# Performance work log

Measured on AMD Instinct MI355X. Metric: run time of the kernel, lower is better.

Reference implementation:

```python
import jax, jax.numpy as jnp
import numpy as np

GRID_SIZE = 5
SPLINE_ORDER = 3
NUM_BASIS = GRID_SIZE + SPLINE_ORDER  # 8


def _make_grid(in_features):
    # efficient-kan style uniform extended grid over [-1, 1]
    h = 2.0 / GRID_SIZE
    g = jnp.arange(-SPLINE_ORDER, GRID_SIZE + SPLINE_ORDER + 1, dtype=jnp.float32) * h - 1.0
    return jnp.broadcast_to(g, (in_features, g.shape[0]))  # [in, 12]


def _b_splines(x, grid):
    # x: [..., in], grid: [in, G]; returns [..., in, NUM_BASIS] via Cox-de Boor
    xe = x[..., None]
    bases = ((xe >= grid[:, :-1]) & (xe < grid[:, 1:])).astype(x.dtype)
    for k in range(1, SPLINE_ORDER + 1):
        left = (xe - grid[:, :-(k + 1)]) / (grid[:, k:-1] - grid[:, :-(k + 1)]) * bases[..., :-1]
        right = (grid[:, k + 1:] - xe) / (grid[:, k + 1:] - grid[:, 1:-k]) * bases[..., 1:]
        bases = left + right
    return bases


def kan_linear(x, bw, sw):
    # bw: [out, in], sw: [out, in, NUM_BASIS]
    base = jnp.matmul(jax.nn.silu(x), bw.T)
    spl = _b_splines(x, _make_grid(bw.shape[1]))
    spline = jnp.einsum('...ik,oik->...o', spl, sw)
    return base + spline


def kan2(x, bw1, sw1, bw2, sw2):
    return kan_linear(kan_linear(x, bw1, sw1), bw2, sw2)


def _att_matrix(q, bw1, sw1, bw2, sw2):
    n, h = q.shape
    pairs = jnp.concatenate([
        jnp.broadcast_to(q[:, None, :], (n, n, h)),
        jnp.broadcast_to(q[None, :, :], (n, n, h)),
    ], axis=-1)  # [n, n, 2h]
    return kan2(pairs, bw1, sw1, bw2, sw2)[..., 0]  # [n, n]


def setup_inputs() -> dict:
    key = jax.random.key(0)
    ks = jax.random.split(key, 32)
    n, h, m = 384, 32, 50

    def rn(k, shape, s=1.0):
        return jax.random.normal(k, shape, dtype=jnp.float32) * s

    inp = {
        'x': rn(ks[0], (n, h)),
        'y': rn(ks[1], (n, h)),
        'target': rn(ks[2], (n, h)),
        'bias': rn(ks[3], (1,), 0.1),
    }
    i = 4
    for pre in ('x', 'y', 't'):
        din = 2 * h
        inp[pre + '1bw'] = rn(ks[i], (m, din), 0.1)
        inp[pre + '1sw'] = rn(ks[i + 1], (m, din, NUM_BASIS), 0.1)
        inp[pre + '2bw'] = rn(ks[i + 2], (1, m), 0.1)
        inp[pre + '2sw'] = rn(ks[i + 3], (1, m, NUM_BASIS), 0.1)
        i += 4
    inp['f1bw'] = rn(ks[i], (m, 3 * h), 0.1)
    inp['f1sw'] = rn(ks[i + 1], (m, 3 * h, NUM_BASIS), 0.1)
    inp['f2bw'] = rn(ks[i + 2], (3, m), 0.1)
    inp['f2sw'] = rn(ks[i + 3], (3, m, NUM_BASIS), 0.1)
    i += 4
    inp['l1bw'] = rn(ks[i], (h, h), 0.1)
    inp['l1sw'] = rn(ks[i + 1], (h, h, NUM_BASIS), 0.1)
    inp['l2bw'] = rn(ks[i + 2], (h, h), 0.1)
    inp['l2sw'] = rn(ks[i + 3], (h, h, NUM_BASIS), 0.1)
    return inp


def reference(x, y, target, bias,
              x1bw, x1sw, x2bw, x2sw,
              y1bw, y1sw, y2bw, y2sw,
              t1bw, t1sw, t2bw, t2sw,
              f1bw, f1sw, f2bw, f2sw,
              l1bw, l1sw, l2bw, l2sw):
    xA = _att_matrix(x, x1bw, x1sw, x2bw, x2sw)
    yA = _att_matrix(y, y1bw, y1sw, y2bw, y2sw)
    tA = _att_matrix(target, t1bw, t1sw, t2bw, t2sw)

    # dynamic modal fusion weights
    feats = jnp.concatenate([x.mean(0, keepdims=True), y.mean(0, keepdims=True),
                             target.mean(0, keepdims=True)], axis=-1)  # [1, 3h]
    w = jax.nn.softmax(kan2(feats, f1bw, f1sw, f2bw, f2sw), axis=-1)[0]  # [3]

    fusion_att = w[0] * xA + w[1] * yA + w[2] * tA + bias
    fusion_att = jax.nn.softmax(fusion_att, axis=-1)
    target_att = jnp.matmul(fusion_att, target)  # dropout is identity at eval
    y1 = jax.nn.relu(kan_linear(target_att, l1bw, l1sw))
    y2 = jax.nn.relu(kan_linear(y1, l2bw, l2sw))
    return y2
```

## Files before the change

### kernel.cpp

```cpp
#include <hip/hip_runtime.h>

#define NN 384
#define HH 32
#define MM 50

__device__ __forceinline__ float fastRcp(float x) { return __builtin_amdgcn_rcpf(x); }

__device__ __forceinline__ void featEval(float x, float& sil, int& kb, float b[4]) {
  sil = x * fastRcp(1.0f + __expf(-x));
  const float u  = (x + 1.0f) * 2.5f;
  const float fu = floorf(u);
  const bool valid = (fu >= -3.0f) && (fu <= 7.0f);
  const float s = valid ? (1.0f / 6.0f) : 0.0f;
  kb = valid ? (int)fu : 100;
  const float tt = u - fu;
  const float t2 = tt * tt, t3 = t2 * tt, omt = 1.0f - tt;
  b[0] = omt * omt * omt * s;
  b[1] = (3.0f * t3 - 6.0f * t2 + 4.0f) * s;
  b[2] = (-3.0f * t3 + 3.0f * t2 + 3.0f * tt + 1.0f) * s;
  b[3] = t3 * s;
}

__device__ __forceinline__ float waveReduce(float v) {
#pragma unroll
  for (int off = 32; off > 0; off >>= 1) v += __shfl_down(v, off);
  return v;
}

__device__ __forceinline__ float dot4(float4 a, float4 b) {
  float r = a.x * b.x;
  r = fmaf(a.y, b.y, r);
  r = fmaf(a.z, b.z, r);
  r = fmaf(a.w, b.w, r);
  return r;
}

__global__ __launch_bounds__(384) void stageA_kernel(
    const float* __restrict__ x, const float* __restrict__ y, const float* __restrict__ tg,
    const float* __restrict__ xbw, const float* __restrict__ xsw,
    const float* __restrict__ ybw, const float* __restrict__ ysw,
    const float* __restrict__ tbw, const float* __restrict__ tsw,
    const float* __restrict__ f1bw, const float* __restrict__ f1sw,
    const float* __restrict__ f2bw, const float* __restrict__ f2sw,
    float* __restrict__ A, float* __restrict__ Bt, float* __restrict__ wout)
{
  const int tid = threadIdx.x;
  const int lane = tid & 63, w = tid >> 6;
  const int i = blockIdx.x;
  const int m = blockIdx.y;
  const int half = blockIdx.z;

  if (i < NN) {
    __shared__ float bas[HH * 8];
    __shared__ float sil[HH];
    const float* q  = (m == 0) ? x   : ((m == 1) ? y   : tg);
    const float* bw = (m == 0) ? xbw : ((m == 1) ? ybw : tbw);
    const float* sw = (m == 0) ? xsw : ((m == 1) ? ysw : tsw);
    const int cb = half * HH;

    if (tid < HH * 8) bas[tid] = 0.0f;
    __syncthreads();
    if (tid < HH) {
      float b[4]; float s; int kb;
      featEval(q[i * HH + tid], s, kb, b);
      sil[tid] = s;
#pragma unroll
      for (int r = 0; r < 4; ++r) {
        const int k = kb + r;
        if ((unsigned)k < 8u) bas[tid * 8 + k] = b[r];
      }
    }
    __syncthreads();

    const float4* bas4 = (const float4*)bas;
    const float4 bb = bas4[lane];
    const float sl = (lane < HH) ? sil[lane] : 0.0f;
#pragma unroll 2
    for (int o = w; o < MM; o += 6) {
      const float4 wv4 = ((const float4*)(sw + ((size_t)(o * 2 * HH + cb) << 3)))[lane];
      const float bwv = (lane < HH) ? bw[o * 2 * HH + cb + lane] : 0.0f;
      float acc = dot4(wv4, bb);
      acc = fmaf(bwv, sl, acc);
      acc = waveReduce(acc);
      if (lane == 0) {
        if (half == 0) A[((size_t)m * NN + i) * MM + o] = acc;
        else           Bt[((size_t)m * MM + o) * NN + i] = acc;
      }
    }
    return;
  }

  if (m != 0 || half != 0) return;
  {
    __shared__ float4 part4[3][8][16];
    __shared__ float sil96[96];
    __shared__ float bas768[96 * 8];
    __shared__ float z1[MM];
    __shared__ float sil2[MM];
    __shared__ float bas400[MM * 8];
    __shared__ float s3[3];

    {
      const int mm = tid >> 7;
      const int sub = tid & 127;
      const int q4 = sub >> 4;
      const int prt = sub & 15;
      const float* src = (mm == 0) ? x : ((mm == 1) ? y : tg);
      const float4* s4 = (const float4*)src;
      float4 a = make_float4(0.f, 0.f, 0.f, 0.f);
      for (int r = prt; r < NN; r += 16) {
        const float4 v = s4[r * 8 + q4];
        a.x += v.x; a.y += v.y; a.z += v.z; a.w += v.w;
      }
      part4[mm][q4][prt] = a;
    }
    for (int idx = tid; idx < 96 * 8; idx += 384) bas768[idx] = 0.0f;
    for (int idx = tid; idx < MM * 8; idx += 384) bas400[idx] = 0.0f;
    __syncthreads();

    if (tid < 96) {
      const int mm = tid >> 5, col = tid & 31;
      const int q4 = col >> 2, comp = col & 3;
      const float* pp = (const float*)&part4[mm][q4][0];
      float v = 0.0f;
#pragma unroll
      for (int prt = 0; prt < 16; ++prt) v += pp[prt * 4 + comp];
      const float fv = v * (1.0f / NN);
      float b[4]; float s; int kb;
      featEval(fv, s, kb, b);
      sil96[tid] = s;
#pragma unroll
      for (int r = 0; r < 4; ++r) {
        const int k = kb + r;
        if ((unsigned)k < 8u) bas768[tid * 8 + k] = b[r];
      }
    }
    __syncthreads();

    {
      const float4* bas4 = (const float4*)bas768;
      for (int o = w; o < MM; o += 6) {
        const float4* sp4 = (const float4*)(f1sw + (size_t)o * (96 * 8));
        float acc = 0.0f;
#pragma unroll
        for (int r = 0; r < 3; ++r)
          acc += dot4(sp4[lane + 64 * r], bas4[lane + 64 * r]);
#pragma unroll
        for (int r = 0; r < 2; ++r) {
          const int e = lane + 64 * r;
          if (e < 96) acc = fmaf(f1bw[o * 96 + e], sil96[e], acc);
        }
        acc = waveReduce(acc);
        if (lane == 0) z1[o] = acc;
      }
    }
    __syncthreads();

    if (tid < MM) {
      float b[4]; float s; int kb;
      featEval(z1[tid], s, kb, b);
      sil2[tid] = s;
#pragma unroll
      for (int r = 0; r < 4; ++r) {
        const int k = kb + r;
        if ((unsigned)k < 8u) bas400[tid * 8 + k] = b[r];
      }
    }
    __syncthreads();

    if (w < 3) {
      const float4* bas4 = (const float4*)bas400;
      const float4* sp4 = (const float4*)(f2sw + (size_t)w * (MM * 8));
      float acc = 0.0f;
#pragma unroll
      for (int r = 0; r < 2; ++r) {
        const int f = lane + 64 * r;
        if (f < MM * 2) acc += dot4(sp4[f], bas4[f]);
      }
      if (lane < MM) acc = fmaf(f2bw[w * MM + lane], sil2[lane], acc);
      acc = waveReduce(acc);
      if (lane == 0) s3[w] = acc;
    }
    __syncthreads();

    if (tid == 0) {
      const float mx = fmaxf(s3[0], fmaxf(s3[1], s3[2]));
      const float e0 = __expf(s3[0] - mx), e1 = __expf(s3[1] - mx), e2 = __expf(s3[2] - mx);
      const float inv = fastRcp(e0 + e1 + e2);
      wout[0] = e0 * inv; wout[1] = e1 * inv; wout[2] = e2 * inv;
    }
  }
}

__global__ __launch_bounds__(384) void score_kernel(
    const float* __restrict__ A, const float* __restrict__ Bt,
    const float* __restrict__ x2bw, const float* __restrict__ y2bw, const float* __restrict__ t2bw,
    const float* __restrict__ x2sw, const float* __restrict__ y2sw, const float* __restrict__ t2sw,
    float* __restrict__ Sp)
{
  __shared__ float sA[MM];
  __shared__ float sBW[MM];
  __shared__ float4 herm[43];
  __shared__ float4 coefC[MM][43];
  const int tid = threadIdx.x;
  const int i = blockIdx.x;
  const int m = blockIdx.y;
  const float* bsrc = (m == 0) ? x2bw : ((m == 1) ? y2bw : t2bw);
  const float* ssrc = (m == 0) ? x2sw : ((m == 1) ? y2sw : t2sw);

  if (tid < MM) {
    sA[tid]  = A[((size_t)m * NN + i) * MM + tid];
    sBW[tid] = bsrc[tid];
  }
  if (tid >= 64 && tid < 64 + 43) {
    const int c = tid - 64;
    float4 h;
    if (c == 0) {
      h = make_float4(0.f, 0.f, 0.f, 0.f);
    } else if (c == 42) {
      h = make_float4(8.2f, 0.4f, 0.f, 0.f);
    } else {
      const float z0 = -8.2f + (float)(c - 1) * 0.4f;
      const float z1 = z0 + 0.4f;
      const float s0 = fastRcp(1.0f + __expf(-z0));
      const float s1 = fastRcp(1.0f + __expf(-z1));
      const float p0 = z0 * s0, p1 = z1 * s1;
      const float m0 = 0.4f * (s0 * (1.0f + z0 * (1.0f - s0)));
      const float m1 = 0.4f * (s1 * (1.0f + z1 * (1.0f - s1)));
      h.x = p0;
      h.y = m0;
      h.z = 3.0f * (p1 - p0) - 2.0f * m0 - m1;
      h.w = 2.0f * (p0 - p1) + m0 + m1;
    }
    herm[c] = h;
  }
  __syncthreads();

  for (int idx = tid; idx < MM * 43; idx += 384) {
    const int k = idx / 43, cc = idx - k * 43;
    const float bwk = sBW[k];
    const float4 H = herm[cc];
    float4 C = make_float4(bwk * H.x, bwk * H.y, bwk * H.z, bwk * H.w);
    if (cc >= 16 && cc <= 26) {
      const int j = cc - 16;
      float p[4];
#pragma unroll
      for (int r = 0; r < 4; ++r) {
        const int pi = j + r - 3;
        p[r] = ((unsigned)pi < 8u) ? ssrc[k * 8 + pi] : 0.0f;
      }
      C.x += (p[0] + 4.0f * p[1] + p[2]) * (1.0f / 6.0f);
      C.y += (p[2] - p[0]) * 0.5f;
      C.z += (p[0] - 2.0f * p[1] + p[2]) * 0.5f;
      C.w += (p[3] - p[0]) * (1.0f / 6.0f) + (p[1] - p[2]) * 0.5f;
    }
    coefC[k][cc] = C;
  }
  __syncthreads();

#define KAN_EVAL(zz, kk, accv)                                          \
  {                                                                     \
    const float z_ = (zz);                                              \
    const float u_ = fmaf(z_, 2.5f, 20.5f);                             \
    const float fu_ = floorf(u_);                                       \
    const float cu_ = fminf(fmaxf(fu_, -1.0f), 41.0f);                  \
    const float t_ = u_ - cu_;                                          \
    const int cc_ = (int)cu_ + 1;                                       \
    const float4 C_ = coefC[kk][cc_];                                   \
    accv += fmaf(t_, fmaf(t_, fmaf(t_, C_.w, C_.z), C_.y), C_.x);       \
  }

  const float* BtBase = Bt + (size_t)m * MM * NN + tid;
  float acc0 = 0.0f, acc1 = 0.0f;
  float za = BtBase[0];
  float zb = BtBase[NN];
  float zc = BtBase[2 * NN];
  float zd = BtBase[3 * NN];
#pragma unroll 5
  for (int k = 0; k < MM; k += 2) {
    float ze = 0.0f, zf = 0.0f;
    if (k + 5 < MM) {
      ze = BtBase[(size_t)(k + 4) * NN];
      zf = BtBase[(size_t)(k + 5) * NN];
    }
    KAN_EVAL(sA[k] + za,     k,     acc0);
    KAN_EVAL(sA[k + 1] + zb, k + 1, acc1);
    za = zc; zb = zd; zc = ze; zd = zf;
  }
#undef KAN_EVAL

  Sp[((size_t)m * NN + i) * NN + tid] = acc0 + acc1;
}

__global__ __launch_bounds__(384) void row_kernel(
    const float* __restrict__ Sp, const float* __restrict__ wv, const float* __restrict__ bias,
    const float* __restrict__ tg,
    const float* __restrict__ l1bw, const float* __restrict__ l1sw,
    const float* __restrict__ l2bw, const float* __restrict__ l2sw,
    float* __restrict__ out)
{
  __shared__ float p[NN];
  __shared__ float redm[6], reds[6];
  __shared__ float part[12][HH];
  __shared__ float ta[HH];
  __shared__ float basF[HH * 8];
  __shared__ float silF[HH];
  __shared__ float y1v[HH];
  const int tid = threadIdx.x;
  const int lane = tid & 63, w = tid >> 6;
  const int i = blockIdx.x;

  float stot = bias[0];
  stot = fmaf(wv[0], Sp[(size_t)i * NN + tid], stot);
  stot = fmaf(wv[1], Sp[((size_t)NN + i) * NN + tid], stot);
  stot = fmaf(wv[2], Sp[((size_t)2 * NN + i) * NN + tid], stot);

  float v = stot;
#pragma unroll
  for (int off = 32; off > 0; off >>= 1) v = fmaxf(v, __shfl_down(v, off));
  if (lane == 0) redm[w] = v;
  __syncthreads();
  float mx = redm[0];
#pragma unroll
  for (int ww = 1; ww < 6; ++ww) mx = fmaxf(mx, redm[ww]);
  const float e = __expf(stot - mx);
  p[tid] = e;
  float sv = e;
#pragma unroll
  for (int off = 32; off > 0; off >>= 1) sv += __shfl_down(sv, off);
  if (lane == 0) reds[w] = sv;
  __syncthreads();
  const float ssum = reds[0] + reds[1] + reds[2] + reds[3] + reds[4] + reds[5];
  const float inv = 1.0f / ssum;

  const int d = tid & 31, g = tid >> 5;
  float acc2 = 0.0f;
  for (int s2 = 0; s2 < 32; ++s2) {
    const int j = g * 32 + s2;
    acc2 = fmaf(p[j], tg[j * HH + d], acc2);
  }
  part[g][d] = acc2;
  if (tid < HH * 8) basF[tid] = 0.0f;
  __syncthreads();
  if (tid < HH) {
    float a = 0.0f;
#pragma unroll
    for (int gg = 0; gg < 12; ++gg) a += part[gg][tid];
    ta[tid] = a * inv;
  }
  __syncthreads();

  if (tid < HH) {
    float b[4]; float s; int kb;
    featEval(ta[tid], s, kb, b);
    silF[tid] = s;
#pragma unroll
    for (int r = 0; r < 4; ++r) {
      const int k = kb + r;
      if ((unsigned)k < 8u) basF[tid * 8 + k] = b[r];
    }
  }
  __syncthreads();
  {
    const float4 bb = ((const float4*)basF)[lane];
    for (int o = w; o < HH; o += 6) {
      const float4* sp4 = (const float4*)(l1sw + ((size_t)o << 8));
      float acc = dot4(sp4[lane], bb);
      if (lane < HH) acc = fmaf(l1bw[o * HH + lane], silF[lane], acc);
      acc = waveReduce(acc);
      if (lane == 0) y1v[o] = fmaxf(acc, 0.0f);
    }
  }
  __syncthreads();
  if (tid < HH * 8) basF[tid] = 0.0f;
  __syncthreads();
  if (tid < HH) {
    float b[4]; float s; int kb;
    featEval(y1v[tid], s, kb, b);
    silF[tid] = s;
#pragma unroll
    for (int r = 0; r < 4; ++r) {
      const int k = kb + r;
      if ((unsigned)k < 8u) basF[tid * 8 + k] = b[r];
    }
  }
  __syncthreads();
  {
    const float4 bb = ((const float4*)basF)[lane];
    for (int o = w; o < HH; o += 6) {
      const float4* sp4 = (const float4*)(l2sw + ((size_t)o << 8));
      float acc = dot4(sp4[lane], bb);
      if (lane < HH) acc = fmaf(l2bw[o * HH + lane], silF[lane], acc);
      acc = waveReduce(acc);
      if (lane == 0) out[i * HH + o] = fmaxf(acc, 0.0f);
    }
  }
}

extern "C" void kernel_launch(void* const* d_in, const int* in_sizes, int n_in,
                              void* d_out, int out_size, void* d_ws, size_t ws_size,
                              hipStream_t stream)
{
  const float* x    = (const float*)d_in[0];
  const float* y    = (const float*)d_in[1];
  const float* tg   = (const float*)d_in[2];
  const float* bias = (const float*)d_in[3];
  const float* x1bw = (const float*)d_in[4];
  const float* x1sw = (const float*)d_in[5];
  const float* x2bw = (const float*)d_in[6];
  const float* x2sw = (const float*)d_in[7];
  const float* y1bw = (const float*)d_in[8];
  const float* y1sw = (const float*)d_in[9];
  const float* y2bw = (const float*)d_in[10];
  const float* y2sw = (const float*)d_in[11];
  const float* t1bw = (const float*)d_in[12];
  const float* t1sw = (const float*)d_in[13];
  const float* t2bw = (const float*)d_in[14];
  const float* t2sw = (const float*)d_in[15];
  const float* f1bw = (const float*)d_in[16];
  const float* f1sw = (const float*)d_in[17];
  const float* f2bw = (const float*)d_in[18];
  const float* f2sw = (const float*)d_in[19];
  const float* l1bw = (const float*)d_in[20];
  const float* l1sw = (const float*)d_in[21];
  const float* l2bw = (const float*)d_in[22];
  const float* l2sw = (const float*)d_in[23];
  float* out = (float*)d_out;

  float* ws = (float*)d_ws;
  float* A  = ws;
  float* Bt = ws + 3 * NN * MM;
  float* Sp = ws + 6 * NN * MM;
  float* wv = Sp + 3 * NN * NN;

  stageA_kernel<<<dim3(NN + 1, 3, 2), 384, 0, stream>>>(
      x, y, tg, x1bw, x1sw, y1bw, y1sw, t1bw, t1sw,
      f1bw, f1sw, f2bw, f2sw, A, Bt, wv);
  score_kernel<<<dim3(NN, 3), 384, 0, stream>>>(A, Bt, x2bw, y2bw, t2bw,
                                                x2sw, y2sw, t2sw, Sp);
  row_kernel<<<NN, 384, 0, stream>>>(Sp, wv, bias, tg, l1bw, l1sw, l2bw, l2sw, out);
}
```

Baseline: 46.25 us.

## Fuse score and row kernels; precompute second-layer coefficient tables in stageA

```diff
diff --git a/kernel.cpp b/kernel.cpp
--- a/kernel.cpp
+++ b/kernel.cpp
@@ -35,14 +35,54 @@
   return r;
 }
 
+__device__ __forceinline__ float4 combinedCoef(int cc, float bwk,
+                                               const float* __restrict__ ssrc, int k) {
+  float4 H;
+  if (cc == 0) {
+    H = make_float4(0.f, 0.f, 0.f, 0.f);
+  } else if (cc == 42) {
+    H = make_float4(8.2f, 0.4f, 0.f, 0.f);
+  } else {
+    const float z0 = -8.2f + (float)(cc - 1) * 0.4f;
+    const float z1 = z0 + 0.4f;
+    const float s0 = fastRcp(1.0f + __expf(-z0));
+    const float s1 = fastRcp(1.0f + __expf(-z1));
+    const float p0 = z0 * s0, p1 = z1 * s1;
+    const float m0 = 0.4f * (s0 * (1.0f + z0 * (1.0f - s0)));
+    const float m1 = 0.4f * (s1 * (1.0f + z1 * (1.0f - s1)));
+    H.x = p0;
+    H.y = m0;
+    H.z = 3.0f * (p1 - p0) - 2.0f * m0 - m1;
+    H.w = 2.0f * (p0 - p1) + m0 + m1;
+  }
+  float4 C = make_float4(bwk * H.x, bwk * H.y, bwk * H.z, bwk * H.w);
+  if (cc >= 16 && cc <= 26) {
+    const int j = cc - 16;
+    float p[4];
+#pragma unroll
+    for (int r = 0; r < 4; ++r) {
+      const int pi = j + r - 3;
+      p[r] = ((unsigned)pi < 8u) ? ssrc[k * 8 + pi] : 0.0f;
+    }
+    C.x += (p[0] + 4.0f * p[1] + p[2]) * (1.0f / 6.0f);
+    C.y += (p[2] - p[0]) * 0.5f;
+    C.z += (p[0] - 2.0f * p[1] + p[2]) * 0.5f;
+    C.w += (p[3] - p[0]) * (1.0f / 6.0f) + (p[1] - p[2]) * 0.5f;
+  }
+  return C;
+}
+
 __global__ __launch_bounds__(384) void stageA_kernel(
     const float* __restrict__ x, const float* __restrict__ y, const float* __restrict__ tg,
     const float* __restrict__ xbw, const float* __restrict__ xsw,
     const float* __restrict__ ybw, const float* __restrict__ ysw,
     const float* __restrict__ tbw, const float* __restrict__ tsw,
+    const float* __restrict__ x2bw, const float* __restrict__ y2bw, const float* __restrict__ t2bw,
+    const float* __restrict__ x2sw, const float* __restrict__ y2sw, const float* __restrict__ t2sw,
     const float* __restrict__ f1bw, const float* __restrict__ f1sw,
     const float* __restrict__ f2bw, const float* __restrict__ f2sw,
-    float* __restrict__ A, float* __restrict__ Bt, float* __restrict__ wout)
+    float* __restrict__ A, float* __restrict__ Bt, float* __restrict__ wout,
+    float4* __restrict__ tbl4)
 {
   const int tid = threadIdx.x;
   const int lane = tid & 63, w = tid >> 6;
@@ -90,7 +130,17 @@
     return;
   }
 
-  if (m != 0 || half != 0) return;
+  if (half == 1) {
+    const float* bsrc = (m == 0) ? x2bw : ((m == 1) ? y2bw : t2bw);
+    const float* ssrc = (m == 0) ? x2sw : ((m == 1) ? y2sw : t2sw);
+    for (int idx = tid; idx < MM * 43; idx += 384) {
+      const int k = idx / 43, cc = idx - k * 43;
+      tbl4[(size_t)m * (MM * 43) + idx] = combinedCoef(cc, bsrc[k], ssrc, k);
+    }
+    return;
+  }
+  if (m != 0) return;
+
   {
     __shared__ float4 part4[3][8][16];
     __shared__ float sil96[96];
@@ -192,71 +242,37 @@
   }
 }
 
-__global__ __launch_bounds__(384) void score_kernel(
+__global__ __launch_bounds__(384) void scoreRow_kernel(
     const float* __restrict__ A, const float* __restrict__ Bt,
-    const float* __restrict__ x2bw, const float* __restrict__ y2bw, const float* __restrict__ t2bw,
-    const float* __restrict__ x2sw, const float* __restrict__ y2sw, const float* __restrict__ t2sw,
-    float* __restrict__ Sp)
+    const float4* __restrict__ tbl4,
+    const float* __restrict__ wv, const float* __restrict__ bias,
+    const float* __restrict__ tg,
+    const float* __restrict__ l1bw, const float* __restrict__ l1sw,
+    const float* __restrict__ l2bw, const float* __restrict__ l2sw,
+    float* __restrict__ out)
 {
-  __shared__ float sA[MM];
-  __shared__ float sBW[MM];
-  __shared__ float4 herm[43];
+  __shared__ float sA[3][MM];
   __shared__ float4 coefC[MM][43];
+  __shared__ float swvb[4];
+  __shared__ float p[NN];
+  __shared__ float redm[6], reds[6];
+  __shared__ float part[12][HH];
+  __shared__ float ta[HH];
+  __shared__ float basF[HH * 8];
+  __shared__ float silF[HH];
+  __shared__ float y1v[HH];
+
   const int tid = threadIdx.x;
+  const int lane = tid & 63, w = tid >> 6;
   const int i = blockIdx.x;
-  const int m = blockIdx.y;
-  const float* bsrc = (m == 0) ? x2bw : ((m == 1) ? y2bw : t2bw);
-  const float* ssrc = (m == 0) ? x2sw : ((m == 1) ? y2sw : t2sw);
-
-  if (tid < MM) {
-    sA[tid]  = A[((size_t)m * NN + i) * MM + tid];
-    sBW[tid] = bsrc[tid];
-  }
-  if (tid >= 64 && tid < 64 + 43) {
-    const int c = tid - 64;
-    float4 h;
-    if (c == 0) {
-      h = make_float4(0.f, 0.f, 0.f, 0.f);
-    } else if (c == 42) {
-      h = make_float4(8.2f, 0.4f, 0.f, 0.f);
-    } else {
-      const float z0 = -8.2f + (float)(c - 1) * 0.4f;
-      const float z1 = z0 + 0.4f;
-      const float s0 = fastRcp(1.0f + __expf(-z0));
-      const float s1 = fastRcp(1.0f + __expf(-z1));
-      const float p0 = z0 * s0, p1 = z1 * s1;
-      const float m0 = 0.4f * (s0 * (1.0f + z0 * (1.0f - s0)));
-      const float m1 = 0.4f * (s1 * (1.0f + z1 * (1.0f - s1)));
-      h.x = p0;
-      h.y = m0;
-      h.z = 3.0f * (p1 - p0) - 2.0f * m0 - m1;
-      h.w = 2.0f * (p0 - p1) + m0 + m1;
-    }
-    herm[c] = h;
-  }
-  __syncthreads();
-
-  for (int idx = tid; idx < MM * 43; idx += 384) {
-    const int k = idx / 43, cc = idx - k * 43;
-    const float bwk = sBW[k];
-    const float4 H = herm[cc];
-    float4 C = make_float4(bwk * H.x, bwk * H.y, bwk * H.z, bwk * H.w);
-    if (cc >= 16 && cc <= 26) {
-      const int j = cc - 16;
-      float p[4];
-#pragma unroll
-      for (int r = 0; r < 4; ++r) {
-        const int pi = j + r - 3;
-        p[r] = ((unsigned)pi < 8u) ? ssrc[k * 8 + pi] : 0.0f;
-      }
-      C.x += (p[0] + 4.0f * p[1] + p[2]) * (1.0f / 6.0f);
-      C.y += (p[2] - p[0]) * 0.5f;
-      C.z += (p[0] - 2.0f * p[1] + p[2]) * 0.5f;
-      C.w += (p[3] - p[0]) * (1.0f / 6.0f) + (p[1] - p[2]) * 0.5f;
-    }
-    coefC[k][cc] = C;
-  }
-  __syncthreads();
+
+  if (tid < 3 * MM) {
+    const int m = tid / MM, k = tid - m * MM;
+    sA[m][k] = A[((size_t)m * NN + i) * MM + k];
+  }
+  if (tid == 0) { swvb[0] = wv[0]; swvb[1] = wv[1]; swvb[2] = wv[2]; swvb[3] = bias[0]; }
+
+  float stot = 0.0f;
 
 #define KAN_EVAL(zz, kk, accv)                                          \
   {                                                                     \
@@ -270,50 +286,38 @@
     accv += fmaf(t_, fmaf(t_, fmaf(t_, C_.w, C_.z), C_.y), C_.x);       \
   }
 
-  const float* BtBase = Bt + (size_t)m * MM * NN + tid;
-  float acc0 = 0.0f, acc1 = 0.0f;
-  float za = BtBase[0];
-  float zb = BtBase[NN];
-  float zc = BtBase[2 * NN];
-  float zd = BtBase[3 * NN];
+#pragma unroll 1
+  for (int m = 0; m < 3; ++m) {
+    __syncthreads();
+    {
+      float4* dst = &coefC[0][0];
+      const float4* src = tbl4 + (size_t)m * (MM * 43);
+      for (int idx = tid; idx < MM * 43; idx += 384) dst[idx] = src[idx];
+    }
+    __syncthreads();
+
+    const float* BtBase = Bt + (size_t)m * MM * NN + tid;
+    float acc0 = 0.0f, acc1 = 0.0f;
+    float za = BtBase[0];
+    float zb = BtBase[NN];
+    float zc = BtBase[2 * NN];
+    float zd = BtBase[3 * NN];
 #pragma unroll 5
-  for (int k = 0; k < MM; k += 2) {
-    float ze = 0.0f, zf = 0.0f;
-    if (k + 5 < MM) {
-      ze = BtBase[(size_t)(k + 4) * NN];
-      zf = BtBase[(size_t)(k + 5) * NN];
-    }
-    KAN_EVAL(sA[k] + za,     k,     acc0);
-    KAN_EVAL(sA[k + 1] + zb, k + 1, acc1);
-    za = zc; zb = zd; zc = ze; zd = zf;
+    for (int k = 0; k < MM; k += 2) {
+      float ze = 0.0f, zf = 0.0f;
+      if (k + 5 < MM) {
+        ze = BtBase[(size_t)(k + 4) * NN];
+        zf = BtBase[(size_t)(k + 5) * NN];
+      }
+      KAN_EVAL(sA[m][k] + za,     k,     acc0);
+      KAN_EVAL(sA[m][k + 1] + zb, k + 1, acc1);
+      za = zc; zb = zd; zc = ze; zd = zf;
+    }
+    const float accm = acc0 + acc1;
+    if (m == 0) stot = fmaf(swvb[0], accm, swvb[3]);
+    else        stot = fmaf(swvb[m], accm, stot);
   }
 #undef KAN_EVAL
-
-  Sp[((size_t)m * NN + i) * NN + tid] = acc0 + acc1;
-}
-
-__global__ __launch_bounds__(384) void row_kernel(
-    const float* __restrict__ Sp, const float* __restrict__ wv, const float* __restrict__ bias,
-    const float* __restrict__ tg,
-    const float* __restrict__ l1bw, const float* __restrict__ l1sw,
-    const float* __restrict__ l2bw, const float* __restrict__ l2sw,
-    float* __restrict__ out)
-{
-  __shared__ float p[NN];
-  __shared__ float redm[6], reds[6];
-  __shared__ float part[12][HH];
-  __shared__ float ta[HH];
-  __shared__ float basF[HH * 8];
-  __shared__ float silF[HH];
-  __shared__ float y1v[HH];
-  const int tid = threadIdx.x;
-  const int lane = tid & 63, w = tid >> 6;
-  const int i = blockIdx.x;
-
-  float stot = bias[0];
-  stot = fmaf(wv[0], Sp[(size_t)i * NN + tid], stot);
-  stot = fmaf(wv[1], Sp[((size_t)NN + i) * NN + tid], stot);
-  stot = fmaf(wv[2], Sp[((size_t)2 * NN + i) * NN + tid], stot);
 
   float v = stot;
 #pragma unroll
@@ -430,13 +434,13 @@
   float* ws = (float*)d_ws;
   float* A  = ws;
   float* Bt = ws + 3 * NN * MM;
-  float* Sp = ws + 6 * NN * MM;
-  float* wv = Sp + 3 * NN * NN;
+  float* wv = ws + 6 * NN * MM;
+  float4* tbl4 = (float4*)(ws + 6 * NN * MM + 4);
 
   stageA_kernel<<<dim3(NN + 1, 3, 2), 384, 0, stream>>>(
       x, y, tg, x1bw, x1sw, y1bw, y1sw, t1bw, t1sw,
-      f1bw, f1sw, f2bw, f2sw, A, Bt, wv);
-  score_kernel<<<dim3(NN, 3), 384, 0, stream>>>(A, Bt, x2bw, y2bw, t2bw,
-                                                x2sw, y2sw, t2sw, Sp);
-  row_kernel<<<NN, 384, 0, stream>>>(Sp, wv, bias, tg, l1bw, l1sw, l2bw, l2sw, out);
-}
+      x2bw, y2bw, t2bw, x2sw, y2sw, t2sw,
+      f1bw, f1sw, f2bw, f2sw, A, Bt, wv, tbl4);
+  scoreRow_kernel<<<NN, 384, 0, stream>>>(
+      A, Bt, tbl4, wv, bias, tg, l1bw, l1sw, l2bw, l2sw, out);
+}
```

Result: no change. 46.98 us (+1.6%).
